# Kernel optimization log

Hardware: AMD Instinct MI355X
Metric: run time of the kernel (lower is better)

## Reference

```python
import jax, jax.numpy as jnp
import numpy as np

B, T, D = 4, 8192, 1024
H = 8
DK = D // H          # head qk dim = 128
DV = D // H          # head v dim = 128
I = 2816             # MLP intermediate size
K = 4                # short conv size
C = 64               # retention chunk size
GATE_EPS = 1e-5      # norm_eps for g_norm_swish_gate
RMS_EPS = 1e-6       # rms_norm_eps for layer norms


def rmsnorm(x, w, eps):
    var = jnp.mean(jnp.square(x), axis=-1, keepdims=True)
    return x * jax.lax.rsqrt(var + eps) * w


def short_conv(x, w):
    # causal depthwise conv1d (kernel K) + silu; x: [B,T,Ch], w: [Ch,K]
    xp = jnp.pad(x, ((0, 0), (K - 1, 0), (0, 0)))
    y = xp[:, 0:T, :] * w[:, 0]
    for k in range(1, K):
        y = y + xp[:, k:k + T, :] * w[:, k]
    return jax.nn.silu(y)


def rope(x):
    # flash-attn style non-interleaved rotary; x: [B,T,H,Dk]
    d2 = x.shape[-1] // 2
    inv_freq = 1.0 / (10000.0 ** (jnp.arange(d2, dtype=jnp.float32) / d2))
    f = jnp.arange(x.shape[1], dtype=jnp.float32)[:, None] * inv_freq[None, :]  # [T,d2]
    cos = jnp.cos(f)[None, :, None, :]
    sin = jnp.sin(f)[None, :, None, :]
    x1, x2 = x[..., :d2], x[..., d2:]
    return jnp.concatenate([x1 * cos - x2 * sin, x1 * sin + x2 * cos], axis=-1)


def retention(q, k, v):
    # chunked RetNet retention. q,k: [B,T,H,DK], v: [B,T,H,DV]
    gamma = 1.0 - jnp.exp2(-5.0 - jnp.arange(H, dtype=jnp.float32))  # [H]
    lg = jnp.log(gamma)
    nc = T // C
    idx = jnp.arange(C, dtype=jnp.float32)
    expo = idx[:, None] - idx[None, :]                                # i-j
    mask = jnp.where(expo >= 0, jnp.exp(lg[:, None, None] * expo), 0.0)  # [H,C,C]
    cross = jnp.exp(lg[:, None] * (idx + 1.0))                        # gamma^{i+1}, [H,C]
    kdec = jnp.exp(lg[:, None] * (C - 1.0 - idx))                     # gamma^{C-1-i}, [H,C]
    cdec = jnp.exp(lg * C)                                            # gamma^C, [H]

    scale = DK ** -0.5
    qc = (q * scale).reshape(B, nc, C, H, DK).transpose(1, 0, 3, 2, 4)  # [nc,B,H,C,DK]
    kc = k.reshape(B, nc, C, H, DK).transpose(1, 0, 3, 2, 4)
    vc = v.reshape(B, nc, C, H, DV).transpose(1, 0, 3, 2, 4)

    def body(S, blk):
        qb, kb, vb = blk  # [B,H,C,D]
        att = jnp.einsum('bhid,bhjd->bhij', qb, kb) * mask
        o = jnp.einsum('bhij,bhje->bhie', att, vb) \
            + jnp.einsum('bhid,bhde->bhie', qb * cross[:, :, None], S)
        S = S * cdec[:, None, None] \
            + jnp.einsum('bhid,bhie->bhde', kb * kdec[:, :, None], vb)
        return S, o

    S0 = jnp.zeros((B, H, DK, DV), q.dtype)
    _, o = jax.lax.scan(body, S0, (qc, kc, vc))  # [nc,B,H,C,DV]
    return o.transpose(1, 0, 3, 2, 4).reshape(B, T, H, DV)


def setup_inputs() -> dict:
    key = jax.random.key(0)
    ks = jax.random.split(key, 16)
    s = 0.02
    return {
        'hidden_states': jax.random.normal(ks[0], (B, T, D), jnp.float32),
        'ln1_w': jnp.ones((D,), jnp.float32),
        'ln2_w': jnp.ones((D,), jnp.float32),
        'wq': jax.random.normal(ks[1], (D, D), jnp.float32) * s,
        'wk': jax.random.normal(ks[2], (D, D), jnp.float32) * s,
        'wv': jax.random.normal(ks[3], (D, D), jnp.float32) * s,
        'wg': jax.random.normal(ks[4], (D, D), jnp.float32) * s,
        'wo': jax.random.normal(ks[5], (D, D), jnp.float32) * s,
        'conv_q_w': jax.random.normal(ks[6], (D, K), jnp.float32) * 0.3,
        'conv_k_w': jax.random.normal(ks[7], (D, K), jnp.float32) * 0.3,
        'conv_v_w': jax.random.normal(ks[8], (D, K), jnp.float32) * 0.3,
        'gnorm_w': jnp.ones((DV,), jnp.float32),
        'w_gate': jax.random.normal(ks[9], (D, I), jnp.float32) * s,
        'w_up': jax.random.normal(ks[10], (D, I), jnp.float32) * s,
        'w_down': jax.random.normal(ks[11], (I, D), jnp.float32) * s,
    }


def reference(hidden_states, ln1_w, ln2_w, wq, wk, wv, wg, wo,
              conv_q_w, conv_k_w, conv_v_w, gnorm_w, w_gate, w_up, w_down):
    # --- attention block ---
    res = hidden_states
    x = rmsnorm(hidden_states, ln1_w, RMS_EPS)
    q = short_conv(x @ wq, conv_q_w)
    k = short_conv(x @ wk, conv_k_w)
    v = short_conv(x @ wv, conv_v_w)
    q = rope(q.reshape(B, T, H, DK))
    k = rope(k.reshape(B, T, H, DK))
    v = v.reshape(B, T, H, DV)
    o = retention(q, k, v)                              # [B,T,H,DV]
    g = (x @ wg).reshape(B, T, H, DV)
    o = rmsnorm(o, gnorm_w, GATE_EPS) * jax.nn.silu(g)  # fused RMSNorm + swish gate
    h = res + o.reshape(B, T, D) @ wo
    # --- MLP block (SwiGLU) ---
    res = h
    y = rmsnorm(h, ln2_w, RMS_EPS)
    y = (jax.nn.silu(y @ w_gate) * (y @ w_up)) @ w_down
    return res + y
```

## Files before the change

kernel.cpp:

```cpp
#include <hip/hip_runtime.h>

typedef unsigned short u16;
typedef float f32x4 __attribute__((ext_vector_type(4)));
typedef short bf16x8 __attribute__((ext_vector_type(8)));

constexpr int Tc = 8192;

#define DEVINL __device__ __forceinline__

DEVINL float b2f(u16 u) { union { unsigned i; float f; } v; v.i = ((unsigned)u) << 16; return v.f; }
DEVINL u16 f2b(float f) {
    union { float f; unsigned i; } v; v.f = f;
    unsigned r = v.i + 0x7fffu + ((v.i >> 16) & 1u);
    return (u16)(r >> 16);
}
DEVINL float silu_f(float x) { return x / (1.f + __expf(-x)); }

#define GLDS(gp, lp) __builtin_amdgcn_global_load_lds((const __attribute__((address_space(1))) void*)(gp), (__attribute__((address_space(3))) void*)(lp), 16, 0, 0)

__global__ void wtrans(const float* __restrict__ in, u16* __restrict__ out, int R, int C)
{
    __shared__ float tile[32][33];
    const int bx = blockIdx.x * 32, by = blockIdx.y * 32;
    const int tx = threadIdx.x, ty = threadIdx.y;
#pragma unroll
    for (int j = 0; j < 32; j += 8)
        tile[ty + j][tx] = in[(size_t)(by + ty + j) * C + bx + tx];
    __syncthreads();
#pragma unroll
    for (int j = 0; j < 32; j += 8)
        out[(size_t)(bx + ty + j) * R + by + tx] = f2b(tile[tx][ty + j]);
}

__global__ __launch_bounds__(256)
void rmsnorm_bf16(const float* __restrict__ x, const float* __restrict__ w, u16* __restrict__ out)
{
    __shared__ float red[256];
    const int tid = threadIdx.x;
    const size_t row = blockIdx.x;
    const float4 xv = ((const float4*)(x + row * 1024))[tid];
    float s = xv.x * xv.x + xv.y * xv.y + xv.z * xv.z + xv.w * xv.w;
    red[tid] = s;
    __syncthreads();
#pragma unroll
    for (int o = 128; o > 0; o >>= 1) {
        if (tid < o) red[tid] += red[tid + o];
        __syncthreads();
    }
    const float rinv = rsqrtf(red[0] * (1.f / 1024.f) + 1e-6f);
    const float4 wv = ((const float4*)w)[tid];
    ushort4 pk = make_ushort4(f2b(xv.x * rinv * wv.x), f2b(xv.y * rinv * wv.y),
                              f2b(xv.z * rinv * wv.z), f2b(xv.w * rinv * wv.w));
    ((ushort4*)(out + row * 1024))[tid] = pk;
}

template <int EPI>
__global__ __launch_bounds__(256)
void gemm_bf16(const u16* __restrict__ A, const u16* __restrict__ Bt,
               void* __restrict__ Out, const float* __restrict__ Res,
               const u16* __restrict__ Other, int N, int K)
{
    __shared__ __align__(16) u16 lsA[128 * 64];
    __shared__ __align__(16) u16 lsB[128 * 64];
    const int tid = threadIdx.x;
    const int wave = tid >> 6, lane = tid & 63;
    const int quad = lane >> 4, l15 = lane & 15;
    const int mBlk = blockIdx.y * 128, nBlk = blockIdx.x * 128;
    const int wm = (wave >> 1) * 64, wn = (wave & 1) * 64;

    f32x4 acc[4][4] = {};

    const int sRow = tid >> 3;
    const int sCol = (tid & 7) * 8;
    const u16* gA = A + (size_t)(mBlk + sRow) * K + sCol;
    const u16* gB = Bt + (size_t)(nBlk + sRow) * K + sCol;
    u16* lA = lsA + wave * 512;
    u16* lB = lsB + wave * 512;

    for (int k0 = 0; k0 < K; k0 += 64) {
        __syncthreads();
#pragma unroll
        for (int i = 0; i < 4; ++i) {
            GLDS(gA + (size_t)i * 32 * K + k0, lA + i * 2048);
            GLDS(gB + (size_t)i * 32 * K + k0, lB + i * 2048);
        }
        __syncthreads();
#pragma unroll
        for (int ks = 0; ks < 2; ++ks) {
            const int ko = ks * 32 + quad * 8;
            bf16x8 af[4], bfr[4];
#pragma unroll
            for (int mt = 0; mt < 4; ++mt) af[mt] = *(const bf16x8*)&lsA[(wm + mt * 16 + l15) * 64 + ko];
#pragma unroll
            for (int nt = 0; nt < 4; ++nt) bfr[nt] = *(const bf16x8*)&lsB[(wn + nt * 16 + l15) * 64 + ko];
#pragma unroll
            for (int mt = 0; mt < 4; ++mt)
#pragma unroll
                for (int nt = 0; nt < 4; ++nt)
                    acc[mt][nt] = __builtin_amdgcn_mfma_f32_16x16x32_bf16(af[mt], bfr[nt], acc[mt][nt], 0, 0, 0);
        }
    }
#pragma unroll
    for (int mt = 0; mt < 4; ++mt)
#pragma unroll
        for (int nt = 0; nt < 4; ++nt)
#pragma unroll
            for (int r = 0; r < 4; ++r) {
                const int row = mBlk + wm + mt * 16 + quad * 4 + r;
                const int col = nBlk + wn + nt * 16 + l15;
                const size_t idx = (size_t)row * N + col;
                const float vacc = acc[mt][nt][r];
                if (EPI == 0) {
                    ((u16*)Out)[idx] = f2b(vacc);
                } else if (EPI == 1) {
                    ((float*)Out)[idx] = vacc + Res[idx];
                } else {
                    const float g = b2f(Other[idx]);
                    ((u16*)Out)[idx] = f2b(silu_f(g) * vacc);
                }
            }
}

__global__ __launch_bounds__(256)
void retA(const u16* __restrict__ qkv, const float* __restrict__ cwk,
          const float* __restrict__ cwv, u16* __restrict__ S)
{
    __shared__ __align__(16) u16 kpre[67 * 128];
    __shared__ __align__(16) u16 vpre[67 * 128];
    __shared__ __align__(16) u16 lk[64 * 128];
    __shared__ __align__(16) u16 lv[64 * 128];
    const int blk = blockIdx.x;
    const int n = blk & 127, h = blk >> 7;
    const int tid = threadIdx.x;
    const int t0 = n * 64;
    const float lg2 = log2f(1.f - exp2f(-5.f - (float)h));
    for (int idx = tid; idx < 2144; idx += 256) {
        const int r = idx >> 5;
        const int c4 = (idx & 31) * 4;
        const int t = t0 - 3 + r;
        ushort4 kz = make_ushort4(0, 0, 0, 0), vz = kz;
        if (t >= 0) {
            const size_t rb = (size_t)t * 3072 + h * 128 + c4;
            kz = *(const ushort4*)&qkv[rb + 1024];
            vz = *(const ushort4*)&qkv[rb + 2048];
        }
        *(ushort4*)&kpre[idx * 4] = kz;
        *(ushort4*)&vpre[idx * 4] = vz;
    }
    __syncthreads();
#pragma unroll
    for (int w = 0; w < 16; ++w) {
        const int item = tid + w * 256;
        const int i = item >> 6, dd = item & 63;
        float k1 = 0, k2 = 0, v1 = 0, v2 = 0;
#pragma unroll
        for (int j = 0; j < 4; ++j) {
            const int r = (i + j) * 128;
            k1 += b2f(kpre[r + dd]) * cwk[(h * 128 + dd) * 4 + j];
            k2 += b2f(kpre[r + dd + 64]) * cwk[(h * 128 + dd + 64) * 4 + j];
            v1 += b2f(vpre[r + dd]) * cwv[(h * 128 + dd) * 4 + j];
            v2 += b2f(vpre[r + dd + 64]) * cwv[(h * 128 + dd + 64) * 4 + j];
        }
        k1 = silu_f(k1); k2 = silu_f(k2); v1 = silu_f(v1); v2 = silu_f(v2);
        const float invf = exp2f(-(float)dd * (13.287712379549449f / 64.f));
        float sn, cs;
        sincosf((float)(t0 + i) * invf, &sn, &cs);
        lk[i * 128 + dd] = f2b(k1 * cs - k2 * sn);
        lk[i * 128 + dd + 64] = f2b(k1 * sn + k2 * cs);
        lv[i * 128 + dd] = f2b(v1);
        lv[i * 128 + dd + 64] = f2b(v2);
    }
    __syncthreads();
    const int e0 = (tid >> 3) * 4, d0 = (tid & 7) * 16;
    float acc[4][16] = {};
    for (int i = 0; i < 64; ++i) {
        const float kdec = exp2f(lg2 * (float)(63 - i));
        float kk[16];
#pragma unroll
        for (int c4 = 0; c4 < 4; ++c4) {
            const ushort4 kv = *(const ushort4*)&lk[i * 128 + d0 + c4 * 4];
            kk[c4 * 4 + 0] = b2f(kv.x); kk[c4 * 4 + 1] = b2f(kv.y);
            kk[c4 * 4 + 2] = b2f(kv.z); kk[c4 * 4 + 3] = b2f(kv.w);
        }
        const ushort4 vv4 = *(const ushort4*)&lv[i * 128 + e0];
        float vv[4] = { b2f(vv4.x) * kdec, b2f(vv4.y) * kdec, b2f(vv4.z) * kdec, b2f(vv4.w) * kdec };
#pragma unroll
        for (int j = 0; j < 4; ++j)
#pragma unroll
            for (int c = 0; c < 16; ++c) acc[j][c] += vv[j] * kk[c];
    }
    const size_t base = (size_t)blk * 16384;
#pragma unroll
    for (int j = 0; j < 4; ++j)
#pragma unroll
        for (int c = 0; c < 16; c += 4) {
            ushort4 pk = make_ushort4(f2b(acc[j][c]), f2b(acc[j][c + 1]), f2b(acc[j][c + 2]), f2b(acc[j][c + 3]));
            *(ushort4*)&S[base + (size_t)(e0 + j) * 128 + d0 + c] = pk;
        }
}

__global__ __launch_bounds__(256)
void retScan(u16* __restrict__ S)
{
    const int g = blockIdx.x * 256 + threadIdx.x;
    const int el = g & 16383;
    const int bh = g >> 14;
    const float lg2 = log2f(1.f - exp2f(-5.f - (float)bh));
    const float cdec = exp2f(lg2 * 64.f);
    float run = 0.f;
    const size_t p = (size_t)bh * (128 * 16384) + el;
    u16 nxt = S[p];
    for (int n = 0; n < 128; ++n) {
        const float z = b2f(nxt);
        if (n < 127) nxt = S[p + (size_t)(n + 1) * 16384];
        S[p + (size_t)n * 16384] = f2b(run);
        run = run * cdec + z;
    }
}

__global__ __launch_bounds__(256)
void retB(const u16* __restrict__ qkv, const u16* __restrict__ S,
          const float* __restrict__ cwq, const float* __restrict__ cwk,
          const float* __restrict__ cwv, const float* __restrict__ gnw,
          u16* __restrict__ gio)
{
    __shared__ __align__(16) u16 qpre[67 * 128];
    __shared__ __align__(16) u16 kpre[67 * 128];
    __shared__ __align__(16) u16 vpre[67 * 128];
    __shared__ __align__(16) u16 lq[64 * 128];
    __shared__ __align__(16) u16 lk[64 * 128];
    __shared__ __align__(16) u16 lvt[128 * 72];
    __shared__ __align__(16) u16 latt[64 * 64];
    const int blk = blockIdx.x;
    const int n = blk & 127, h = blk >> 7;
    const int tid = threadIdx.x, wave = tid >> 6, lane = tid & 63;
    const int quad = lane >> 4, l15 = lane & 15;
    const int t0 = n * 64;
    const float lg2 = log2f(1.f - exp2f(-5.f - (float)h));
    const float scale = 0.08838834764831845f;
    for (int idx = tid; idx < 2144; idx += 256) {
        const int r = idx >> 5;
        const int c4 = (idx & 31) * 4;
        const int t = t0 - 3 + r;
        ushort4 qz = make_ushort4(0, 0, 0, 0), kz = qz, vz = qz;
        if (t >= 0) {
            const size_t rb = (size_t)t * 3072 + h * 128 + c4;
            qz = *(const ushort4*)&qkv[rb];
            kz = *(const ushort4*)&qkv[rb + 1024];
            vz = *(const ushort4*)&qkv[rb + 2048];
        }
        *(ushort4*)&qpre[idx * 4] = qz;
        *(ushort4*)&kpre[idx * 4] = kz;
        *(ushort4*)&vpre[idx * 4] = vz;
    }
    __syncthreads();
#pragma unroll
    for (int w = 0; w < 16; ++w) {
        const int item = tid + w * 256;
        const int i = item >> 6, dd = item & 63;
        float q1 = 0, q2 = 0, k1 = 0, k2 = 0, v1 = 0, v2 = 0;
#pragma unroll
        for (int j = 0; j < 4; ++j) {
            const int r = (i + j) * 128;
            const int w1 = (h * 128 + dd) * 4 + j, w2 = (h * 128 + dd + 64) * 4 + j;
            q1 += b2f(qpre[r + dd]) * cwq[w1];
            q2 += b2f(qpre[r + dd + 64]) * cwq[w2];
            k1 += b2f(kpre[r + dd]) * cwk[w1];
            k2 += b2f(kpre[r + dd + 64]) * cwk[w2];
            v1 += b2f(vpre[r + dd]) * cwv[w1];
            v2 += b2f(vpre[r + dd + 64]) * cwv[w2];
        }
        q1 = silu_f(q1); q2 = silu_f(q2); k1 = silu_f(k1);
        k2 = silu_f(k2); v1 = silu_f(v1); v2 = silu_f(v2);
        const float invf = exp2f(-(float)dd * (13.287712379549449f / 64.f));
        float sn, cs;
        sincosf((float)(t0 + i) * invf, &sn, &cs);
        lq[i * 128 + dd] = f2b((q1 * cs - q2 * sn) * scale);
        lq[i * 128 + dd + 64] = f2b((q1 * sn + q2 * cs) * scale);
        lk[i * 128 + dd] = f2b(k1 * cs - k2 * sn);
        lk[i * 128 + dd + 64] = f2b(k1 * sn + k2 * cs);
        lvt[dd * 72 + i] = f2b(v1);
        lvt[(dd + 64) * 72 + i] = f2b(v2);
    }
    __syncthreads();
    const int iB = wave * 16;
    bf16x8 aq[4];
#pragma unroll
    for (int ks = 0; ks < 4; ++ks) aq[ks] = *(const bf16x8*)&lq[(iB + l15) * 128 + ks * 32 + quad * 8];
#pragma unroll
    for (int jt = 0; jt < 4; ++jt) {
        f32x4 c = {};
#pragma unroll
        for (int ks = 0; ks < 4; ++ks) {
            const bf16x8 bk = *(const bf16x8*)&lk[(jt * 16 + l15) * 128 + ks * 32 + quad * 8];
            c = __builtin_amdgcn_mfma_f32_16x16x32_bf16(aq[ks], bk, c, 0, 0, 0);
        }
#pragma unroll
        for (int r = 0; r < 4; ++r) {
            const int i_ = iB + quad * 4 + r;
            const int j_ = jt * 16 + l15;
            const float v = (i_ >= j_) ? c[r] * exp2f(lg2 * (float)(i_ - j_)) : 0.f;
            latt[i_ * 64 + j_] = f2b(v);
        }
    }
    bf16x8 ax[4];
    {
        const float cross = exp2f(lg2 * (float)(iB + l15 + 1));
#pragma unroll
        for (int ks = 0; ks < 4; ++ks) {
            bf16x8 o;
#pragma unroll
            for (int j = 0; j < 8; ++j) o[j] = (short)f2b(b2f((u16)aq[ks][j]) * cross);
            ax[ks] = o;
        }
    }
    bf16x8 aat[2];
#pragma unroll
    for (int k2 = 0; k2 < 2; ++k2) aat[k2] = *(const bf16x8*)&latt[(iB + l15) * 64 + k2 * 32 + quad * 8];
    const size_t Sb = (size_t)blk * 16384;
    f32x4 oc[8];
#pragma unroll
    for (int et = 0; et < 8; ++et) {
        f32x4 c = {};
#pragma unroll
        for (int k2 = 0; k2 < 2; ++k2) {
            const bf16x8 bv = *(const bf16x8*)&lvt[(et * 16 + l15) * 72 + k2 * 32 + quad * 8];
            c = __builtin_amdgcn_mfma_f32_16x16x32_bf16(aat[k2], bv, c, 0, 0, 0);
        }
#pragma unroll
        for (int ks = 0; ks < 4; ++ks) {
            const bf16x8 bs = *(const bf16x8*)&S[Sb + (size_t)(et * 16 + l15) * 128 + ks * 32 + quad * 8];
            c = __builtin_amdgcn_mfma_f32_16x16x32_bf16(ax[ks], bs, c, 0, 0, 0);
        }
        oc[et] = c;
    }
#pragma unroll
    for (int r = 0; r < 4; ++r) {
        float ss = 0.f;
#pragma unroll
        for (int et = 0; et < 8; ++et) ss += oc[et][r] * oc[et][r];
        ss += __shfl_xor(ss, 1); ss += __shfl_xor(ss, 2);
        ss += __shfl_xor(ss, 4); ss += __shfl_xor(ss, 8);
        const float rinv = rsqrtf(ss * (1.f / 128.f) + 1e-5f);
        const int i_ = iB + quad * 4 + r;
        const size_t row = (size_t)(t0 + i_);
#pragma unroll
        for (int et = 0; et < 8; ++et) {
            const int e = et * 16 + l15;
            const size_t gi = row * 1024 + h * 128 + e;
            const float gv = b2f(gio[gi]);
            gio[gi] = f2b(oc[et][r] * rinv * gnw[e] * silu_f(gv));
        }
    }
}

extern "C" void kernel_launch(void* const* d_in, const int* in_sizes, int n_in,
                              void* d_out, int out_size, void* d_ws, size_t ws_size,
                              hipStream_t stream)
{
    const float* hidden = (const float*)d_in[0];
    const float* ln1 = (const float*)d_in[1];
    const float* ln2 = (const float*)d_in[2];
    const float* wq = (const float*)d_in[3];
    const float* wk = (const float*)d_in[4];
    const float* wv = (const float*)d_in[5];
    const float* wg = (const float*)d_in[6];
    const float* wo = (const float*)d_in[7];
    const float* cq = (const float*)d_in[8];
    const float* ck = (const float*)d_in[9];
    const float* cv = (const float*)d_in[10];
    const float* gnw = (const float*)d_in[11];
    const float* wgate = (const float*)d_in[12];
    const float* wup = (const float*)d_in[13];
    const float* wdown = (const float*)d_in[14];
    float* out = (float*)d_out;

    char* ws = (char*)d_ws;
    u16* W3T = (u16*)(ws + 0);
    u16* WGm = (u16*)(ws + 6291456);
    u16* WOT = (u16*)(ws + 8388608);
    u16* WGT = (u16*)(ws + 10485760);
    u16* WUT = (u16*)(ws + 16252928);
    u16* WDT = (u16*)(ws + 22020096);
    u16* XNb  = (u16*)(ws + 27787264);
    u16* Gb   = (u16*)(ws + 44564480);
    u16* QKVb = (u16*)(ws + 61341696);
    u16* SBb  = (u16*)(ws + 111673344);
    u16* GATEb = (u16*)(ws + 61341696);
    u16* ACTb  = (u16*)(ws + 107479040);

    dim3 tb(32, 8);
    wtrans<<<dim3(32, 32), tb, 0, stream>>>(wq, W3T, 1024, 1024);
    wtrans<<<dim3(32, 32), tb, 0, stream>>>(wk, W3T + 1048576, 1024, 1024);
    wtrans<<<dim3(32, 32), tb, 0, stream>>>(wv, W3T + 2097152, 1024, 1024);
    wtrans<<<dim3(32, 32), tb, 0, stream>>>(wg, WGm, 1024, 1024);
    wtrans<<<dim3(32, 32), tb, 0, stream>>>(wo, WOT, 1024, 1024);
    wtrans<<<dim3(88, 32), tb, 0, stream>>>(wgate, WGT, 1024, 2816);
    wtrans<<<dim3(88, 32), tb, 0, stream>>>(wup, WUT, 1024, 2816);
    wtrans<<<dim3(32, 88), tb, 0, stream>>>(wdown, WDT, 2816, 1024);

    for (int b = 0; b < 4; ++b) {
        const float* hb = hidden + (size_t)b * 8192 * 1024;
        float* ob = out + (size_t)b * 8192 * 1024;
        rmsnorm_bf16<<<8192, 256, 0, stream>>>(hb, ln1, XNb);
        gemm_bf16<0><<<dim3(24, 64), 256, 0, stream>>>(XNb, W3T, QKVb, nullptr, nullptr, 3072, 1024);
        gemm_bf16<0><<<dim3(8, 64), 256, 0, stream>>>(XNb, WGm, Gb, nullptr, nullptr, 1024, 1024);
        retA<<<1024, 256, 0, stream>>>(QKVb, ck, cv, SBb);
        retScan<<<512, 256, 0, stream>>>(SBb);
        retB<<<1024, 256, 0, stream>>>(QKVb, SBb, cq, ck, cv, gnw, Gb);
        gemm_bf16<1><<<dim3(8, 64), 256, 0, stream>>>(Gb, WOT, ob, hb, nullptr, 1024, 1024);
        rmsnorm_bf16<<<8192, 256, 0, stream>>>(ob, ln2, XNb);
        gemm_bf16<0><<<dim3(22, 64), 256, 0, stream>>>(XNb, WGT, GATEb, nullptr, nullptr, 2816, 1024);
        gemm_bf16<2><<<dim3(22, 64), 256, 0, stream>>>(XNb, WUT, ACTb, nullptr, GATEb, 2816, 1024);
        gemm_bf16<1><<<dim3(8, 64), 256, 0, stream>>>(ACTb, WDT, ob, ob, nullptr, 1024, 2816);
    }
}
```

Before: 2.902 ms.

## Share one prefetch LDS buffer across q/k/v phases in retention kernels

The retention kernels retA and retB now stage k, v and q through a single reused shared-memory prefetch buffer, one tensor at a time, instead of three separate buffers. In retB the RoPE sin/cos values are kept in registers and reused between the k and q phases, and launch bounds request two blocks per SM. This cuts LDS use so more blocks can be resident, at the cost of extra barriers and serialized global loads that overlap less.

```diff
diff --git a/kernel.cpp b/kernel.cpp
--- a/kernel.cpp
+++ b/kernel.cpp
@@ -125,8 +125,7 @@
 void retA(const u16* __restrict__ qkv, const float* __restrict__ cwk,
           const float* __restrict__ cwv, u16* __restrict__ S)
 {
-    __shared__ __align__(16) u16 kpre[67 * 128];
-    __shared__ __align__(16) u16 vpre[67 * 128];
+    __shared__ __align__(16) u16 pre[67 * 128];
     __shared__ __align__(16) u16 lk[64 * 128];
     __shared__ __align__(16) u16 lv[64 * 128];
     const int blk = blockIdx.x;
@@ -134,41 +133,57 @@
     const int tid = threadIdx.x;
     const int t0 = n * 64;
     const float lg2 = log2f(1.f - exp2f(-5.f - (float)h));
+
     for (int idx = tid; idx < 2144; idx += 256) {
         const int r = idx >> 5;
         const int c4 = (idx & 31) * 4;
         const int t = t0 - 3 + r;
-        ushort4 kz = make_ushort4(0, 0, 0, 0), vz = kz;
-        if (t >= 0) {
-            const size_t rb = (size_t)t * 3072 + h * 128 + c4;
-            kz = *(const ushort4*)&qkv[rb + 1024];
-            vz = *(const ushort4*)&qkv[rb + 2048];
-        }
-        *(ushort4*)&kpre[idx * 4] = kz;
-        *(ushort4*)&vpre[idx * 4] = vz;
+        ushort4 kz = make_ushort4(0, 0, 0, 0);
+        if (t >= 0) kz = *(const ushort4*)&qkv[(size_t)t * 3072 + 1024 + h * 128 + c4];
+        *(ushort4*)&pre[idx * 4] = kz;
     }
     __syncthreads();
 #pragma unroll
     for (int w = 0; w < 16; ++w) {
         const int item = tid + w * 256;
         const int i = item >> 6, dd = item & 63;
-        float k1 = 0, k2 = 0, v1 = 0, v2 = 0;
+        float k1 = 0, k2 = 0;
 #pragma unroll
         for (int j = 0; j < 4; ++j) {
             const int r = (i + j) * 128;
-            k1 += b2f(kpre[r + dd]) * cwk[(h * 128 + dd) * 4 + j];
-            k2 += b2f(kpre[r + dd + 64]) * cwk[(h * 128 + dd + 64) * 4 + j];
-            v1 += b2f(vpre[r + dd]) * cwv[(h * 128 + dd) * 4 + j];
-            v2 += b2f(vpre[r + dd + 64]) * cwv[(h * 128 + dd + 64) * 4 + j];
-        }
-        k1 = silu_f(k1); k2 = silu_f(k2); v1 = silu_f(v1); v2 = silu_f(v2);
+            k1 += b2f(pre[r + dd]) * cwk[(h * 128 + dd) * 4 + j];
+            k2 += b2f(pre[r + dd + 64]) * cwk[(h * 128 + dd + 64) * 4 + j];
+        }
+        k1 = silu_f(k1); k2 = silu_f(k2);
         const float invf = exp2f(-(float)dd * (13.287712379549449f / 64.f));
         float sn, cs;
         sincosf((float)(t0 + i) * invf, &sn, &cs);
         lk[i * 128 + dd] = f2b(k1 * cs - k2 * sn);
         lk[i * 128 + dd + 64] = f2b(k1 * sn + k2 * cs);
-        lv[i * 128 + dd] = f2b(v1);
-        lv[i * 128 + dd + 64] = f2b(v2);
+    }
+    __syncthreads();
+    for (int idx = tid; idx < 2144; idx += 256) {
+        const int r = idx >> 5;
+        const int c4 = (idx & 31) * 4;
+        const int t = t0 - 3 + r;
+        ushort4 vz = make_ushort4(0, 0, 0, 0);
+        if (t >= 0) vz = *(const ushort4*)&qkv[(size_t)t * 3072 + 2048 + h * 128 + c4];
+        *(ushort4*)&pre[idx * 4] = vz;
+    }
+    __syncthreads();
+#pragma unroll
+    for (int w = 0; w < 16; ++w) {
+        const int item = tid + w * 256;
+        const int i = item >> 6, dd = item & 63;
+        float v1 = 0, v2 = 0;
+#pragma unroll
+        for (int j = 0; j < 4; ++j) {
+            const int r = (i + j) * 128;
+            v1 += b2f(pre[r + dd]) * cwv[(h * 128 + dd) * 4 + j];
+            v2 += b2f(pre[r + dd + 64]) * cwv[(h * 128 + dd + 64) * 4 + j];
+        }
+        lv[i * 128 + dd] = f2b(silu_f(v1));
+        lv[i * 128 + dd + 64] = f2b(silu_f(v2));
     }
     __syncthreads();
     const int e0 = (tid >> 3) * 4, d0 = (tid & 7) * 16;
@@ -218,15 +233,13 @@
     }
 }
 
-__global__ __launch_bounds__(256)
+__global__ __launch_bounds__(256, 2)
 void retB(const u16* __restrict__ qkv, const u16* __restrict__ S,
           const float* __restrict__ cwq, const float* __restrict__ cwk,
           const float* __restrict__ cwv, const float* __restrict__ gnw,
           u16* __restrict__ gio)
 {
-    __shared__ __align__(16) u16 qpre[67 * 128];
-    __shared__ __align__(16) u16 kpre[67 * 128];
-    __shared__ __align__(16) u16 vpre[67 * 128];
+    __shared__ __align__(16) u16 pre[67 * 128];
     __shared__ __align__(16) u16 lq[64 * 128];
     __shared__ __align__(16) u16 lk[64 * 128];
     __shared__ __align__(16) u16 lvt[128 * 72];
@@ -238,51 +251,87 @@
     const int t0 = n * 64;
     const float lg2 = log2f(1.f - exp2f(-5.f - (float)h));
     const float scale = 0.08838834764831845f;
+
     for (int idx = tid; idx < 2144; idx += 256) {
         const int r = idx >> 5;
         const int c4 = (idx & 31) * 4;
         const int t = t0 - 3 + r;
-        ushort4 qz = make_ushort4(0, 0, 0, 0), kz = qz, vz = qz;
-        if (t >= 0) {
-            const size_t rb = (size_t)t * 3072 + h * 128 + c4;
-            qz = *(const ushort4*)&qkv[rb];
-            kz = *(const ushort4*)&qkv[rb + 1024];
-            vz = *(const ushort4*)&qkv[rb + 2048];
-        }
-        *(ushort4*)&qpre[idx * 4] = qz;
-        *(ushort4*)&kpre[idx * 4] = kz;
-        *(ushort4*)&vpre[idx * 4] = vz;
+        ushort4 vz = make_ushort4(0, 0, 0, 0);
+        if (t >= 0) vz = *(const ushort4*)&qkv[(size_t)t * 3072 + 2048 + h * 128 + c4];
+        *(ushort4*)&pre[idx * 4] = vz;
     }
     __syncthreads();
 #pragma unroll
     for (int w = 0; w < 16; ++w) {
         const int item = tid + w * 256;
         const int i = item >> 6, dd = item & 63;
-        float q1 = 0, q2 = 0, k1 = 0, k2 = 0, v1 = 0, v2 = 0;
+        float v1 = 0, v2 = 0;
 #pragma unroll
         for (int j = 0; j < 4; ++j) {
             const int r = (i + j) * 128;
-            const int w1 = (h * 128 + dd) * 4 + j, w2 = (h * 128 + dd + 64) * 4 + j;
-            q1 += b2f(qpre[r + dd]) * cwq[w1];
-            q2 += b2f(qpre[r + dd + 64]) * cwq[w2];
-            k1 += b2f(kpre[r + dd]) * cwk[w1];
-            k2 += b2f(kpre[r + dd + 64]) * cwk[w2];
-            v1 += b2f(vpre[r + dd]) * cwv[w1];
-            v2 += b2f(vpre[r + dd + 64]) * cwv[w2];
-        }
-        q1 = silu_f(q1); q2 = silu_f(q2); k1 = silu_f(k1);
-        k2 = silu_f(k2); v1 = silu_f(v1); v2 = silu_f(v2);
+            v1 += b2f(pre[r + dd]) * cwv[(h * 128 + dd) * 4 + j];
+            v2 += b2f(pre[r + dd + 64]) * cwv[(h * 128 + dd + 64) * 4 + j];
+        }
+        lvt[dd * 72 + i] = f2b(silu_f(v1));
+        lvt[(dd + 64) * 72 + i] = f2b(silu_f(v2));
+    }
+    __syncthreads();
+
+    for (int idx = tid; idx < 2144; idx += 256) {
+        const int r = idx >> 5;
+        const int c4 = (idx & 31) * 4;
+        const int t = t0 - 3 + r;
+        ushort4 kz = make_ushort4(0, 0, 0, 0);
+        if (t >= 0) kz = *(const ushort4*)&qkv[(size_t)t * 3072 + 1024 + h * 128 + c4];
+        *(ushort4*)&pre[idx * 4] = kz;
+    }
+    __syncthreads();
+    float snr[16], csr[16];
+#pragma unroll
+    for (int w = 0; w < 16; ++w) {
+        const int item = tid + w * 256;
+        const int i = item >> 6, dd = item & 63;
+        float k1 = 0, k2 = 0;
+#pragma unroll
+        for (int j = 0; j < 4; ++j) {
+            const int r = (i + j) * 128;
+            k1 += b2f(pre[r + dd]) * cwk[(h * 128 + dd) * 4 + j];
+            k2 += b2f(pre[r + dd + 64]) * cwk[(h * 128 + dd + 64) * 4 + j];
+        }
+        k1 = silu_f(k1); k2 = silu_f(k2);
         const float invf = exp2f(-(float)dd * (13.287712379549449f / 64.f));
-        float sn, cs;
-        sincosf((float)(t0 + i) * invf, &sn, &cs);
-        lq[i * 128 + dd] = f2b((q1 * cs - q2 * sn) * scale);
-        lq[i * 128 + dd + 64] = f2b((q1 * sn + q2 * cs) * scale);
-        lk[i * 128 + dd] = f2b(k1 * cs - k2 * sn);
-        lk[i * 128 + dd + 64] = f2b(k1 * sn + k2 * cs);
-        lvt[dd * 72 + i] = f2b(v1);
-        lvt[(dd + 64) * 72 + i] = f2b(v2);
-    }
-    __syncthreads();
+        sincosf((float)(t0 + i) * invf, &snr[w], &csr[w]);
+        lk[i * 128 + dd] = f2b(k1 * csr[w] - k2 * snr[w]);
+        lk[i * 128 + dd + 64] = f2b(k1 * snr[w] + k2 * csr[w]);
+    }
+    __syncthreads();
+
+    for (int idx = tid; idx < 2144; idx += 256) {
+        const int r = idx >> 5;
+        const int c4 = (idx & 31) * 4;
+        const int t = t0 - 3 + r;
+        ushort4 qz = make_ushort4(0, 0, 0, 0);
+        if (t >= 0) qz = *(const ushort4*)&qkv[(size_t)t * 3072 + h * 128 + c4];
+        *(ushort4*)&pre[idx * 4] = qz;
+    }
+    __syncthreads();
+#pragma unroll
+    for (int w = 0; w < 16; ++w) {
+        const int item = tid + w * 256;
+        const int i = item >> 6, dd = item & 63;
+        float q1 = 0, q2 = 0;
+#pragma unroll
+        for (int j = 0; j < 4; ++j) {
+            const int r = (i + j) * 128;
+            q1 += b2f(pre[r + dd]) * cwq[(h * 128 + dd) * 4 + j];
+            q2 += b2f(pre[r + dd + 64]) * cwq[(h * 128 + dd + 64) * 4 + j];
+        }
+        q1 = silu_f(q1); q2 = silu_f(q2);
+        lq[i * 128 + dd] = f2b((q1 * csr[w] - q2 * snr[w]) * scale);
+        lq[i * 128 + dd + 64] = f2b((q1 * snr[w] + q2 * csr[w]) * scale);
+    }
+    __syncthreads();
+
     const int iB = wave * 16;
     bf16x8 aq[4];
 #pragma unroll
```

After: 2.496 ms. 14.0% less time.
